# Optimization experiments

Measured on AMD Instinct MI355X. Metric: run time of the kernel, lower is better.

## Reference

```python
import jax, jax.numpy as jnp
import numpy as np

D_MODEL = 1024
N_HEADS = 16
D_HEAD = 64
NEG = -1000000000.0


def setup_inputs() -> dict:
    key = jax.random.key(0)
    k1, k2, k3 = jax.random.split(key, 3)
    B, T = 2, 2048
    x = jax.random.normal(k1, (B, T, D_MODEL), dtype=jnp.float32)
    # qkv_proj: Linear(d_model, 3*H*D, bias=False) -> weight (3*H*D, d_model)
    w_qkv = jax.random.normal(k2, (3 * N_HEADS * D_HEAD, D_MODEL), dtype=jnp.float32) * (D_MODEL ** -0.5)
    # o_proj: Linear(H*D, d_model, bias=False) -> weight (d_model, H*D)
    w_o = jax.random.normal(k3, (D_MODEL, N_HEADS * D_HEAD), dtype=jnp.float32) * ((N_HEADS * D_HEAD) ** -0.5)
    return {"x": x, "w_qkv": w_qkv, "w_o": w_o}


def reference(x, w_qkv, w_o):
    B, T, _ = x.shape
    H, D = N_HEADS, D_HEAD
    scale = D ** -0.5
    qkv = jnp.einsum('btm,nm->btn', x, w_qkv).reshape(B, T, 3, H, D)
    q, k, v = qkv[:, :, 0], qkv[:, :, 1], qkv[:, :, 2]  # (B,T,H,D)
    # scores: (B,H,T,T)
    attn = jnp.einsum('bqhd,bkhd->bhqk', q, k) * scale
    causal = jnp.tril(jnp.ones((T, T), dtype=x.dtype))
    attn = attn + (1.0 - causal) * NEG
    attn = jax.nn.softmax(attn, axis=-1)
    out = jnp.einsum('bhqk,bkhd->bqhd', attn, v).reshape(B, T, H * D)
    out = jnp.einsum('btn,mn->btm', out, w_o)
    return (out, k, v)
```

## Files before the change

kernel.cpp:

```cpp
#include <hip/hip_runtime.h>
#include <cstdint>

typedef unsigned short u16;
typedef __bf16 bf16x8 __attribute__((ext_vector_type(8)));
typedef float f32x4 __attribute__((ext_vector_type(4)));
typedef short s4 __attribute__((ext_vector_type(4)));

#define T_SEQ 2048
#define NH 16

__device__ __forceinline__ u16 f2bf(float f) {
  union { float f; uint32_t u; } x; x.f = f;
  uint32_t r = (x.u + 0x7fffu + ((x.u >> 16) & 1u)) >> 16;
  return (u16)r;
}

__device__ __forceinline__ uint32_t pk2bf(float a, float b) {
  union { float f; uint32_t u; } x, y; x.f = a; y.f = b;
  uint32_t lo = (x.u + 0x7fffu + ((x.u >> 16) & 1u)) >> 16;
  uint32_t hi = (y.u + 0x7fffu + ((y.u >> 16) & 1u)) >> 16;
  return lo | (hi << 16);
}

__device__ __forceinline__ void cvt8(u16* dst, const float* src) {
  float4 a = *(const float4*)src;
  float4 b = *(const float4*)(src + 4);
  uint4 o;
  o.x = pk2bf(a.x, a.y); o.y = pk2bf(a.z, a.w);
  o.z = pk2bf(b.x, b.y); o.w = pk2bf(b.z, b.w);
  *(uint4*)dst = o;
}

__global__ __launch_bounds__(256) void cvt_all(const float* __restrict__ x,
                                               const float* __restrict__ wq,
                                               const float* __restrict__ wo,
                                               u16* __restrict__ dst) {
  int i = blockIdx.x * 256 + threadIdx.x;
  const float* src; int off;
  if (i < 524288)      { src = x;  off = 0; }
  else if (i < 917504) { src = wq; off = 524288; }
  else                 { src = wo; off = 917504; }
  cvt8(&dst[(size_t)i * 8], &src[(size_t)(i - off) * 8]);
}

__device__ __forceinline__ s4 cvt4(f32x4 v) {
  union { __bf16 b[4]; s4 s; } u;
  u.b[0] = (__bf16)v[0]; u.b[1] = (__bf16)v[1];
  u.b[2] = (__bf16)v[2]; u.b[3] = (__bf16)v[3];
  return u.s;
}

__device__ __forceinline__ f32x4 mfma16(s4 a, s4 b, f32x4 c) {
#if __has_builtin(__builtin_amdgcn_mfma_f32_16x16x16bf16_1k)
  return __builtin_amdgcn_mfma_f32_16x16x16bf16_1k(a, b, c, 0, 0, 0);
#else
  asm("v_mfma_f32_16x16x16_bf16 %0, %1, %2, %0" : "+v"(c) : "v"(a), "v"(b));
  return c;
#endif
}

__device__ __forceinline__ float exp2fast(float x) {
#if __has_builtin(__builtin_amdgcn_exp2f)
  return __builtin_amdgcn_exp2f(x);
#else
  float r; asm("v_exp_f32 %0, %1" : "=v"(r) : "v"(x)); return r;
#endif
}

__device__ __forceinline__ void gl_lds(const u16* g, u16* ldsbase) {
  __builtin_amdgcn_global_load_lds(
      (const __attribute__((address_space(1))) void*)g,
      (__attribute__((address_space(3))) void*)ldsbase, 16, 0, 0);
}

template <bool CF32, bool KV, int WAVES>
__global__ __launch_bounds__(WAVES * 64) void gemm_bt(
    const u16* __restrict__ A, const u16* __restrict__ W,
    void* __restrict__ Cp, float* __restrict__ outk, float* __restrict__ outv,
    u16* __restrict__ vtp, int M, int N, int K) {
  constexpr int NJ = (WAVES == 4) ? 4 : 2;
  constexpr int SI = 16 / WAVES;
  __shared__ __align__(16) u16 As[128 * 64];
  __shared__ __align__(16) u16 Bs[128 * 64];
  const int tid  = threadIdx.x;
  const int bid  = blockIdx.y * gridDim.x + blockIdx.x;
  const int per  = (gridDim.x * gridDim.y) >> 3;
  const int swz  = (bid & 7) * per + (bid >> 3);
  const int n0   = (swz % gridDim.x) * 128;
  const int m0   = (swz / gridDim.x) * 128;
  const int tid_ = tid;
  const int lane = tid_ & 63;
  const int wave = tid_ >> 6;
  const int wm   = (WAVES == 4 ? (wave >> 1) : (wave >> 2)) * 64;
  const int wn   = (WAVES == 4 ? (wave & 1) * 64 : (wave & 3) * 32);
  const int l15  = lane & 15;
  const int quad = lane >> 4;
  const int srow = lane >> 3;
  const int sc   = lane & 7;

  f32x4 acc[4][NJ];
#pragma unroll
  for (int i = 0; i < 4; i++)
#pragma unroll
    for (int j = 0; j < NJ; j++) acc[i][j] = (f32x4){0.f, 0.f, 0.f, 0.f};

  for (int k0 = 0; k0 < K; k0 += 64) {
    __syncthreads();
#pragma unroll
    for (int i = 0; i < SI; i++) {
      int r0  = (i * WAVES + wave) * 8;
      int row = r0 + srow;
      int gc  = (sc ^ (row & 7)) << 3;
      gl_lds(&A[(size_t)(m0 + row) * K + k0 + gc], &As[r0 * 64]);
      gl_lds(&W[(size_t)(n0 + row) * K + k0 + gc], &Bs[r0 * 64]);
    }
    __syncthreads();
#pragma unroll
    for (int kk = 0; kk < 64; kk += 32) {
      bf16x8 af[4], bfr[NJ];
#pragma unroll
      for (int i = 0; i < 4; i++) {
        int arow = wm + i * 16 + l15;
        af[i] = *(const bf16x8*)((const char*)As + arow * 128 +
                                 ((((kk >> 3) + quad) ^ (arow & 7)) << 4));
      }
#pragma unroll
      for (int j = 0; j < NJ; j++) {
        int brow = wn + j * 16 + l15;
        bfr[j] = *(const bf16x8*)((const char*)Bs + brow * 128 +
                                  ((((kk >> 3) + quad) ^ (brow & 7)) << 4));
      }
#pragma unroll
      for (int i = 0; i < 4; i++)
#pragma unroll
        for (int j = 0; j < NJ; j++)
          acc[i][j] = __builtin_amdgcn_mfma_f32_16x16x32_bf16(af[i], bfr[j], acc[i][j], 0, 0, 0);
    }
  }
#pragma unroll
  for (int i = 0; i < 4; i++)
#pragma unroll
    for (int j = 0; j < NJ; j++) {
      const int row0 = m0 + wm + i * 16 + quad * 4;
      const int col  = n0 + wn + j * 16 + l15;
      if constexpr (CF32) {
#pragma unroll
        for (int r = 0; r < 4; r++)
          ((float*)Cp)[(size_t)(row0 + r) * N + col] = acc[i][j][r];
      } else if (KV && col >= 2048) {
        const int hd = col - 2048;
        const int b_ = row0 >> 11, t_ = row0 & 2047;
        uint2 pk;
        pk.x = pk2bf(acc[i][j][0], acc[i][j][1]);
        pk.y = pk2bf(acc[i][j][2], acc[i][j][3]);
        *(uint2*)&vtp[((size_t)(b_ * NH + (hd >> 6)) * 64 + (hd & 63)) * 2048 + t_] = pk;
#pragma unroll
        for (int r = 0; r < 4; r++)
          outv[(size_t)(row0 + r) * 1024 + hd] = acc[i][j][r];
      } else {
#pragma unroll
        for (int r = 0; r < 4; r++) {
          float v = acc[i][j][r];
          ((u16*)Cp)[(size_t)(row0 + r) * N + col] = f2bf(v);
          if constexpr (KV) {
            if (col >= 1024) outk[(size_t)(row0 + r) * 1024 + (col - 1024)] = v;
          }
        }
      }
    }
}

__global__ __launch_bounds__(256) void attn(const u16* __restrict__ qkv,
                                            const u16* __restrict__ vt,
                                            u16* __restrict__ o) {
  __shared__ __align__(16) u16 Ks[3][64 * 64];
  __shared__ __align__(16) u16 Vts[3][64 * 64];

  const int tid  = threadIdx.x;
  const int bh   = blockIdx.y;
  const int b    = bh >> 4, h = bh & 15;
  const int p    = b ? (int)blockIdx.x : 15 - (int)blockIdx.x;
  const int lane = tid & 63, wave = tid >> 6;
  const int grp  = wave >> 1;
  const int half = wave & 1;
  const int l15  = lane & 15, quad = lane >> 4;
  const int srow = lane >> 3, sc = lane & 7;
  const size_t qbase = (size_t)b * T_SEQ * 3072;
  const size_t vbase = (size_t)(b * NH + h) * 64 * 2048;
  const float C = 0.1803368801f;

  const int qt    = 2 * p + 1 - grp;
  const int steps = 2 * p + 2;

  int wq0[2];
  wq0[0] = qt * 64 + half * 32;
  wq0[1] = wq0[0] + 16;

  bf16x8 qf[2][2];
#pragma unroll
  for (int q = 0; q < 2; q++) {
    const u16* qp = &qkv[qbase + (size_t)(wq0[q] + l15) * 3072 + h * 64];
    qf[q][0] = *(const bf16x8*)&qp[quad * 8];
    qf[q][1] = *(const bf16x8*)&qp[32 + quad * 8];
  }

  f32x4 acc_o[2][4];
#pragma unroll
  for (int q = 0; q < 2; q++)
#pragma unroll
    for (int n = 0; n < 4; n++) acc_o[q][n] = (f32x4){0.f, 0.f, 0.f, 0.f};
  float m2run[2] = {-1e30f, -1e30f}, lrun[2] = {0.f, 0.f};

  auto stage = [&](int buf, int kt) {
    const int k0 = kt * 64;
#pragma unroll
    for (int i = 0; i < 2; i++) {
      int r0  = (wave * 2 + i) * 8;
      int row = r0 + srow;
      int gc  = (sc ^ (row & 7)) << 3;
      gl_lds(&qkv[qbase + (size_t)(k0 + row) * 3072 + 1024 + h * 64 + gc], &Ks[buf][r0 * 64]);
      gl_lds(&vt[vbase + (size_t)row * 2048 + k0 + gc], &Vts[buf][r0 * 64]);
    }
  };

  stage(0, 0);
  stage(1, 1);

  for (int s = 0; s < steps; s++) {
    if (s < steps - 1) asm volatile("s_waitcnt vmcnt(4)" ::: "memory");
    else               asm volatile("s_waitcnt vmcnt(0)" ::: "memory");
    __builtin_amdgcn_s_barrier();
    __builtin_amdgcn_sched_barrier(0);

    if (s + 2 < steps) stage((s + 2) % 3, s + 2);

    if (s <= qt) {
      const int cur = s % 3;
      const int k0  = s * 64;

      f32x4 sacc[2][4];
#pragma unroll
      for (int q = 0; q < 2; q++)
#pragma unroll
        for (int j = 0; j < 4; j++) sacc[q][j] = (f32x4){0.f, 0.f, 0.f, 0.f};

      __builtin_amdgcn_s_setprio(1);
#pragma unroll
      for (int j = 0; j < 4; j++) {
        int krow = j * 16 + l15;
        const char* kb = (const char*)&Ks[cur][0] + krow * 128;
        bf16x8 kfa = *(const bf16x8*)(kb + ((quad ^ (krow & 7)) << 4));
        bf16x8 kfb = *(const bf16x8*)(kb + (((4 + quad) ^ (krow & 7)) << 4));
#pragma unroll
        for (int q = 0; q < 2; q++) {
          sacc[q][j] = __builtin_amdgcn_mfma_f32_16x16x32_bf16(kfa, qf[q][0], sacc[q][j], 0, 0, 0);
          sacc[q][j] = __builtin_amdgcn_mfma_f32_16x16x32_bf16(kfb, qf[q][1], sacc[q][j], 0, 0, 0);
        }
      }
      __builtin_amdgcn_s_setprio(0);

      if (s == qt) {
#pragma unroll
        for (int q = 0; q < 2; q++)
#pragma unroll
          for (int j = 0; j < 4; j++)
#pragma unroll
            for (int r = 0; r < 4; r++) {
              int k = k0 + j * 16 + quad * 4 + r;
              if (k > wq0[q] + l15) sacc[q][j][r] = -1e30f;
            }
      }

      s4 pa[2][4];
#pragma unroll
      for (int q = 0; q < 2; q++) {
        float mj[4];
#pragma unroll
        for (int j = 0; j < 4; j++)
          mj[j] = fmaxf(fmaxf(sacc[q][j][0], sacc[q][j][1]),
                        fmaxf(sacc[q][j][2], sacc[q][j][3]));
        float mx = fmaxf(fmaxf(mj[0], mj[1]), fmaxf(mj[2], mj[3]));
        mx = fmaxf(mx, __shfl_xor(mx, 16));
        mx = fmaxf(mx, __shfl_xor(mx, 32));
        const float m2x = mx * C;

        if (!__all(m2x <= m2run[q] + 8.0f)) {
          const float m2new = fmaxf(m2run[q], m2x);
          const float alpha = exp2fast(m2run[q] - m2new);
          lrun[q] *= alpha;
          m2run[q] = m2new;
#pragma unroll
          for (int r = 0; r < 4; r++) {
            float ar = __shfl(alpha, quad * 4 + r);
#pragma unroll
            for (int n = 0; n < 4; n++) acc_o[q][n][r] *= ar;
          }
        }

        const float nm = m2run[q];
        float ts[4];
#pragma unroll
        for (int j = 0; j < 4; j++) {
#pragma unroll
          for (int r = 0; r < 4; r++)
            sacc[q][j][r] = exp2fast(fmaf(sacc[q][j][r], C, -nm));
          ts[j] = (sacc[q][j][0] + sacc[q][j][1]) + (sacc[q][j][2] + sacc[q][j][3]);
        }
        float sum = (ts[0] + ts[1]) + (ts[2] + ts[3]);
        sum += __shfl_xor(sum, 16);
        sum += __shfl_xor(sum, 32);
        lrun[q] += sum;

#pragma unroll
        for (int j = 0; j < 4; j++) pa[q][j] = cvt4(sacc[q][j]);
      }

      __builtin_amdgcn_s_setprio(1);
#pragma unroll
      for (int j = 0; j < 4; j++)
#pragma unroll
        for (int n = 0; n < 4; n++) {
          int vrow = n * 16 + l15;
          int ch = (j * 2 + (quad >> 1)) ^ (vrow & 7);
          const s4 vf = *(const s4*)((const char*)&Vts[cur][0] + vrow * 128 +
                                     (ch << 4) + ((quad & 1) << 3));
#pragma unroll
          for (int q = 0; q < 2; q++)
            acc_o[q][n] = mfma16(pa[q][j], vf, acc_o[q][n]);
        }
      __builtin_amdgcn_s_setprio(0);
    }
  }

#pragma unroll
  for (int q = 0; q < 2; q++) {
    const float linv = 1.0f / lrun[q];
#pragma unroll
    for (int r = 0; r < 4; r++) {
      const float lr = __shfl(linv, quad * 4 + r);
      const int row = wq0[q] + quad * 4 + r;
#pragma unroll
      for (int n = 0; n < 4; n++)
        o[(size_t)(b * T_SEQ + row) * 1024 + h * 64 + n * 16 + l15] =
            f2bf(acc_o[q][n][r] * lr);
    }
  }
}

extern "C" void kernel_launch(void* const* d_in, const int* in_sizes, int n_in,
                              void* d_out, int out_size, void* d_ws, size_t ws_size,
                              hipStream_t stream) {
  const float* x     = (const float*)d_in[0];
  const float* w_qkv = (const float*)d_in[1];
  const float* w_o   = (const float*)d_in[2];
  float* out  = (float*)d_out;
  float* outk = out + (size_t)4194304;
  float* outv = out + (size_t)8388608;

  u16* qkv = (u16*)d_ws;
  u16* vt  = qkv + (size_t)4096 * 3072;
  u16* ao  = vt  + (size_t)4194304;
  u16* xb  = ao  + (size_t)4194304;
  u16* wqb = xb  + (size_t)4194304;
  u16* wob = wqb + (size_t)3145728;

  cvt_all<<<4096, 256, 0, stream>>>(x, w_qkv, w_o, xb);

  gemm_bt<false, true, 4><<<dim3(24, 32), 256, 0, stream>>>(
      xb, wqb, qkv, outk, outv, vt, 4096, 3072, 1024);
  attn<<<dim3(16, 32), 256, 0, stream>>>(qkv, vt, ao);
  gemm_bt<true, false, 8><<<dim3(8, 32), 512, 0, stream>>>(
      ao, wob, out, nullptr, nullptr, nullptr, 4096, 1024, 1024);
}
```

Measured before the change: 218.9 us.

## Double-buffer GEMM LDS tiles and pair mirrored query tiles in attention

The GEMM now double-buffers its A/B LDS tiles, issuing the next tile's global-to-LDS loads before computing the current one, with a single barrier per iteration. The attention kernel now gives each block two mirrored query tiles (pair and 31-pair), one 16-row slice per wave, so every block walks a similar number of causal KV steps. K fragments are loaded once and shared by both tiles, and the short tile's P is zeroed once it is finished. The aim is to hide GEMM load latency and even out causal work across blocks, at the cost of double the GEMM LDS (which may lower occupancy) and some wasted MFMAs on zeroed P.

```diff
diff --git a/kernel.cpp b/kernel.cpp
--- a/kernel.cpp
+++ b/kernel.cpp
@@ -80,17 +80,16 @@
     u16* __restrict__ vtp, int M, int N, int K) {
   constexpr int NJ = (WAVES == 4) ? 4 : 2;
   constexpr int SI = 16 / WAVES;
-  __shared__ __align__(16) u16 As[128 * 64];
-  __shared__ __align__(16) u16 Bs[128 * 64];
+  __shared__ __align__(16) u16 As[2][128 * 64];
+  __shared__ __align__(16) u16 Bs[2][128 * 64];
   const int tid  = threadIdx.x;
   const int bid  = blockIdx.y * gridDim.x + blockIdx.x;
   const int per  = (gridDim.x * gridDim.y) >> 3;
   const int swz  = (bid & 7) * per + (bid >> 3);
   const int n0   = (swz % gridDim.x) * 128;
   const int m0   = (swz / gridDim.x) * 128;
-  const int tid_ = tid;
-  const int lane = tid_ & 63;
-  const int wave = tid_ >> 6;
+  const int lane = tid & 63;
+  const int wave = tid >> 6;
   const int wm   = (WAVES == 4 ? (wave >> 1) : (wave >> 2)) * 64;
   const int wn   = (WAVES == 4 ? (wave & 1) * 64 : (wave & 3) * 32);
   const int l15  = lane & 15;
@@ -104,30 +103,39 @@
 #pragma unroll
     for (int j = 0; j < NJ; j++) acc[i][j] = (f32x4){0.f, 0.f, 0.f, 0.f};
 
-  for (int k0 = 0; k0 < K; k0 += 64) {
-    __syncthreads();
+  auto stage = [&](int d, int k0) {
 #pragma unroll
     for (int i = 0; i < SI; i++) {
       int r0  = (i * WAVES + wave) * 8;
       int row = r0 + srow;
       int gc  = (sc ^ (row & 7)) << 3;
-      gl_lds(&A[(size_t)(m0 + row) * K + k0 + gc], &As[r0 * 64]);
-      gl_lds(&W[(size_t)(n0 + row) * K + k0 + gc], &Bs[r0 * 64]);
-    }
-    __syncthreads();
+      gl_lds(&A[(size_t)(m0 + row) * K + k0 + gc], &As[d][r0 * 64]);
+      gl_lds(&W[(size_t)(n0 + row) * K + k0 + gc], &Bs[d][r0 * 64]);
+    }
+  };
+
+  stage(0, 0);
+  asm volatile("s_waitcnt vmcnt(0)" ::: "memory");
+  __builtin_amdgcn_s_barrier();
+  __builtin_amdgcn_sched_barrier(0);
+
+  const int NT = K >> 6;
+  int cur = 0;
+  for (int t = 0; t < NT; t++) {
+    if (t + 1 < NT) stage(cur ^ 1, (t + 1) * 64);
 #pragma unroll
     for (int kk = 0; kk < 64; kk += 32) {
       bf16x8 af[4], bfr[NJ];
 #pragma unroll
       for (int i = 0; i < 4; i++) {
         int arow = wm + i * 16 + l15;
-        af[i] = *(const bf16x8*)((const char*)As + arow * 128 +
+        af[i] = *(const bf16x8*)((const char*)&As[cur][0] + arow * 128 +
                                  ((((kk >> 3) + quad) ^ (arow & 7)) << 4));
       }
 #pragma unroll
       for (int j = 0; j < NJ; j++) {
         int brow = wn + j * 16 + l15;
-        bfr[j] = *(const bf16x8*)((const char*)Bs + brow * 128 +
+        bfr[j] = *(const bf16x8*)((const char*)&Bs[cur][0] + brow * 128 +
                                   ((((kk >> 3) + quad) ^ (brow & 7)) << 4));
       }
 #pragma unroll
@@ -136,6 +144,10 @@
         for (int j = 0; j < NJ; j++)
           acc[i][j] = __builtin_amdgcn_mfma_f32_16x16x32_bf16(af[i], bfr[j], acc[i][j], 0, 0, 0);
     }
+    asm volatile("s_waitcnt vmcnt(0)" ::: "memory");
+    __builtin_amdgcn_s_barrier();
+    __builtin_amdgcn_sched_barrier(0);
+    cur ^= 1;
   }
 #pragma unroll
   for (int i = 0; i < 4; i++)
@@ -179,22 +191,20 @@
   const int tid  = threadIdx.x;
   const int bh   = blockIdx.y;
   const int b    = bh >> 4, h = bh & 15;
-  const int p    = b ? (int)blockIdx.x : 15 - (int)blockIdx.x;
+  const int pair = b ? (int)blockIdx.x : 15 - (int)blockIdx.x;
   const int lane = tid & 63, wave = tid >> 6;
-  const int grp  = wave >> 1;
-  const int half = wave & 1;
   const int l15  = lane & 15, quad = lane >> 4;
   const int srow = lane >> 3, sc = lane & 7;
   const size_t qbase = (size_t)b * T_SEQ * 3072;
   const size_t vbase = (size_t)(b * NH + h) * 64 * 2048;
   const float C = 0.1803368801f;
 
-  const int qt    = 2 * p + 1 - grp;
-  const int steps = 2 * p + 2;
+  const int qt[2] = {pair, 31 - pair};
+  const int steps = 32 - pair;
 
   int wq0[2];
-  wq0[0] = qt * 64 + half * 32;
-  wq0[1] = wq0[0] + 16;
+  wq0[0] = qt[0] * 64 + wave * 16;
+  wq0[1] = qt[1] * 64 + wave * 16;
 
   bf16x8 qf[2][2];
 #pragma unroll
@@ -234,102 +244,109 @@
 
     if (s + 2 < steps) stage((s + 2) % 3, s + 2);
 
-    if (s <= qt) {
-      const int cur = s % 3;
-      const int k0  = s * 64;
-
-      f32x4 sacc[2][4];
-#pragma unroll
-      for (int q = 0; q < 2; q++)
-#pragma unroll
-        for (int j = 0; j < 4; j++) sacc[q][j] = (f32x4){0.f, 0.f, 0.f, 0.f};
-
-      __builtin_amdgcn_s_setprio(1);
+    const bool aAct = (s <= qt[0]);
+    const int cur = s % 3;
+    const int k0  = s * 64;
+
+    bf16x8 kfr[4][2];
+#pragma unroll
+    for (int j = 0; j < 4; j++) {
+      int krow = j * 16 + l15;
+      const char* kb = (const char*)&Ks[cur][0] + krow * 128;
+      kfr[j][0] = *(const bf16x8*)(kb + ((quad ^ (krow & 7)) << 4));
+      kfr[j][1] = *(const bf16x8*)(kb + (((4 + quad) ^ (krow & 7)) << 4));
+    }
+
+    f32x4 sacc[2][4];
+    __builtin_amdgcn_s_setprio(1);
+#pragma unroll
+    for (int j = 0; j < 4; j++) {
+      sacc[1][j] = (f32x4){0.f, 0.f, 0.f, 0.f};
+      sacc[1][j] = __builtin_amdgcn_mfma_f32_16x16x32_bf16(kfr[j][0], qf[1][0], sacc[1][j], 0, 0, 0);
+      sacc[1][j] = __builtin_amdgcn_mfma_f32_16x16x32_bf16(kfr[j][1], qf[1][1], sacc[1][j], 0, 0, 0);
+    }
+    if (aAct) {
 #pragma unroll
       for (int j = 0; j < 4; j++) {
-        int krow = j * 16 + l15;
-        const char* kb = (const char*)&Ks[cur][0] + krow * 128;
-        bf16x8 kfa = *(const bf16x8*)(kb + ((quad ^ (krow & 7)) << 4));
-        bf16x8 kfb = *(const bf16x8*)(kb + (((4 + quad) ^ (krow & 7)) << 4));
-#pragma unroll
-        for (int q = 0; q < 2; q++) {
-          sacc[q][j] = __builtin_amdgcn_mfma_f32_16x16x32_bf16(kfa, qf[q][0], sacc[q][j], 0, 0, 0);
-          sacc[q][j] = __builtin_amdgcn_mfma_f32_16x16x32_bf16(kfb, qf[q][1], sacc[q][j], 0, 0, 0);
+        sacc[0][j] = (f32x4){0.f, 0.f, 0.f, 0.f};
+        sacc[0][j] = __builtin_amdgcn_mfma_f32_16x16x32_bf16(kfr[j][0], qf[0][0], sacc[0][j], 0, 0, 0);
+        sacc[0][j] = __builtin_amdgcn_mfma_f32_16x16x32_bf16(kfr[j][1], qf[0][1], sacc[0][j], 0, 0, 0);
+      }
+    }
+    __builtin_amdgcn_s_setprio(0);
+
+    s4 pa[2][4];
+#pragma unroll
+    for (int j = 0; j < 4; j++) pa[0][j] = (s4){0, 0, 0, 0};
+
+#pragma unroll
+    for (int q = 0; q < 2; q++) {
+      if (q == 0 && !aAct) continue;
+
+      if (s == qt[q]) {
+#pragma unroll
+        for (int j = 0; j < 4; j++)
+#pragma unroll
+          for (int r = 0; r < 4; r++) {
+            int k = k0 + j * 16 + quad * 4 + r;
+            if (k > wq0[q] + l15) sacc[q][j][r] = -1e30f;
+          }
+      }
+
+      float mj[4];
+#pragma unroll
+      for (int j = 0; j < 4; j++)
+        mj[j] = fmaxf(fmaxf(sacc[q][j][0], sacc[q][j][1]),
+                      fmaxf(sacc[q][j][2], sacc[q][j][3]));
+      float mx = fmaxf(fmaxf(mj[0], mj[1]), fmaxf(mj[2], mj[3]));
+      mx = fmaxf(mx, __shfl_xor(mx, 16));
+      mx = fmaxf(mx, __shfl_xor(mx, 32));
+      const float m2x = mx * C;
+
+      if (!__all(m2x <= m2run[q] + 8.0f)) {
+        const float m2new = fmaxf(m2run[q], m2x);
+        const float alpha = exp2fast(m2run[q] - m2new);
+        lrun[q] *= alpha;
+        m2run[q] = m2new;
+#pragma unroll
+        for (int r = 0; r < 4; r++) {
+          float ar = __shfl(alpha, quad * 4 + r);
+#pragma unroll
+          for (int n = 0; n < 4; n++) acc_o[q][n][r] *= ar;
         }
       }
-      __builtin_amdgcn_s_setprio(0);
-
-      if (s == qt) {
-#pragma unroll
-        for (int q = 0; q < 2; q++)
-#pragma unroll
-          for (int j = 0; j < 4; j++)
-#pragma unroll
-            for (int r = 0; r < 4; r++) {
-              int k = k0 + j * 16 + quad * 4 + r;
-              if (k > wq0[q] + l15) sacc[q][j][r] = -1e30f;
-            }
-      }
-
-      s4 pa[2][4];
-#pragma unroll
-      for (int q = 0; q < 2; q++) {
-        float mj[4];
-#pragma unroll
-        for (int j = 0; j < 4; j++)
-          mj[j] = fmaxf(fmaxf(sacc[q][j][0], sacc[q][j][1]),
-                        fmaxf(sacc[q][j][2], sacc[q][j][3]));
-        float mx = fmaxf(fmaxf(mj[0], mj[1]), fmaxf(mj[2], mj[3]));
-        mx = fmaxf(mx, __shfl_xor(mx, 16));
-        mx = fmaxf(mx, __shfl_xor(mx, 32));
-        const float m2x = mx * C;
-
-        if (!__all(m2x <= m2run[q] + 8.0f)) {
-          const float m2new = fmaxf(m2run[q], m2x);
-          const float alpha = exp2fast(m2run[q] - m2new);
-          lrun[q] *= alpha;
-          m2run[q] = m2new;
-#pragma unroll
-          for (int r = 0; r < 4; r++) {
-            float ar = __shfl(alpha, quad * 4 + r);
-#pragma unroll
-            for (int n = 0; n < 4; n++) acc_o[q][n][r] *= ar;
-          }
-        }
-
-        const float nm = m2run[q];
-        float ts[4];
-#pragma unroll
-        for (int j = 0; j < 4; j++) {
-#pragma unroll
-          for (int r = 0; r < 4; r++)
-            sacc[q][j][r] = exp2fast(fmaf(sacc[q][j][r], C, -nm));
-          ts[j] = (sacc[q][j][0] + sacc[q][j][1]) + (sacc[q][j][2] + sacc[q][j][3]);
-        }
-        float sum = (ts[0] + ts[1]) + (ts[2] + ts[3]);
-        sum += __shfl_xor(sum, 16);
-        sum += __shfl_xor(sum, 32);
-        lrun[q] += sum;
-
-#pragma unroll
-        for (int j = 0; j < 4; j++) pa[q][j] = cvt4(sacc[q][j]);
-      }
-
-      __builtin_amdgcn_s_setprio(1);
-#pragma unroll
-      for (int j = 0; j < 4; j++)
-#pragma unroll
-        for (int n = 0; n < 4; n++) {
-          int vrow = n * 16 + l15;
-          int ch = (j * 2 + (quad >> 1)) ^ (vrow & 7);
-          const s4 vf = *(const s4*)((const char*)&Vts[cur][0] + vrow * 128 +
-                                     (ch << 4) + ((quad & 1) << 3));
-#pragma unroll
-          for (int q = 0; q < 2; q++)
-            acc_o[q][n] = mfma16(pa[q][j], vf, acc_o[q][n]);
-        }
-      __builtin_amdgcn_s_setprio(0);
-    }
+
+      const float nm = m2run[q];
+      float ts[4];
+#pragma unroll
+      for (int j = 0; j < 4; j++) {
+#pragma unroll
+        for (int r = 0; r < 4; r++)
+          sacc[q][j][r] = exp2fast(fmaf(sacc[q][j][r], C, -nm));
+        ts[j] = (sacc[q][j][0] + sacc[q][j][1]) + (sacc[q][j][2] + sacc[q][j][3]);
+      }
+      float sum = (ts[0] + ts[1]) + (ts[2] + ts[3]);
+      sum += __shfl_xor(sum, 16);
+      sum += __shfl_xor(sum, 32);
+      lrun[q] += sum;
+
+#pragma unroll
+      for (int j = 0; j < 4; j++) pa[q][j] = cvt4(sacc[q][j]);
+    }
+
+    __builtin_amdgcn_s_setprio(1);
+#pragma unroll
+    for (int j = 0; j < 4; j++)
+#pragma unroll
+      for (int n = 0; n < 4; n++) {
+        int vrow = n * 16 + l15;
+        int ch = (j * 2 + (quad >> 1)) ^ (vrow & 7);
+        const s4 vf = *(const s4*)((const char*)&Vts[cur][0] + vrow * 128 +
+                                   (ch << 4) + ((quad & 1) << 3));
+        acc_o[1][n] = mfma16(pa[1][j], vf, acc_o[1][n]);
+        acc_o[0][n] = mfma16(pa[0][j], vf, acc_o[0][n]);
+      }
+    __builtin_amdgcn_s_setprio(0);
   }
 
 #pragma unroll
```

Result: faster. 210.1 us (-4.0%).
